# Kernel tuning notes

Hardware: AMD Instinct MI355X
Metric: run time of the kernel (lower is better)

The kernel has to match this reference:

```python
import jax, jax.numpy as jnp
import numpy as np

B, C, R, Cc = 16384, 30, 7, 7

def setup_inputs() -> dict:
    key = jax.random.key(0)
    k1, k2, k3 = jax.random.split(key, 3)
    pred = jax.random.uniform(k1, (B, C, R, Cc), dtype=jnp.float32)
    label = jax.random.uniform(k2, (B, C, R, Cc), dtype=jnp.float32)
    obj = (jax.random.uniform(k3, (B, R, Cc)) > 0.7).astype(jnp.float32)
    label = label.at[:, 4].set(obj)
    return {"pred": pred, "label": label}

def _boxes(t, cols, rows, nrow, ncol, off):
    # t: [b,30,r,c]; channels off..off+3 are (x,y,w,h) relative to cell
    x, y, w, h = t[:, off], t[:, off + 1], t[:, off + 2], t[:, off + 3]
    cx = (x + cols) / ncol
    cy = (y + rows) / nrow
    return cx - w / 2, cy - h / 2, cx + w / 2, cy + h / 2

def _iou(a, b):
    ax1, ay1, ax2, ay2 = a
    bx1, by1, bx2, by2 = b
    iw = jnp.maximum(jnp.minimum(ax2, bx2) - jnp.maximum(ax1, bx1), 0.0)
    ih = jnp.maximum(jnp.minimum(ay2, by2) - jnp.maximum(ay1, by1), 0.0)
    inter = iw * ih
    area_a = (ax2 - ax1) * (ay2 - ay1)
    area_b = (bx2 - bx1) * (by2 - by1)
    return inter / (area_a + area_b - inter + 1e-10)

def reference(pred, label):
    b_size = pred.shape[0]
    nrow, ncol = pred.shape[-2], pred.shape[-1]
    cols = jnp.arange(ncol, dtype=pred.dtype)[None, None, :]  # [1,1,c]
    rows = jnp.arange(nrow, dtype=pred.dtype)[None, :, None]  # [1,r,1]

    bbox1 = _boxes(pred, cols, rows, nrow, ncol, 0)
    bbox2 = _boxes(pred, cols, rows, nrow, ncol, 5)
    lbox = _boxes(label, cols, rows, nrow, ncol, 0)
    iou1 = _iou(bbox1, lbox)  # [b,r,c]
    iou2 = _iou(bbox2, lbox)
    choose1 = iou1 >= iou2

    # coord loss candidates (sum over the 2 xy channels / 2 wh channels)
    coord1 = 5.0 * jnp.sum((pred[:, 0:2] - label[:, 0:2]) ** 2, axis=1) \
           + jnp.sum((jnp.sqrt(pred[:, 2:4]) - jnp.sqrt(label[:, 2:4])) ** 2, axis=1)
    coord2 = 5.0 * jnp.sum((pred[:, 5:7] - label[:, 5:7]) ** 2, axis=1) \
           + jnp.sum((jnp.sqrt(pred[:, 7:9]) - jnp.sqrt(label[:, 7:9])) ** 2, axis=1)

    obj1 = (pred[:, 4] - iou1) ** 2
    obj2 = (pred[:, 9] - iou2) ** 2

    coord = jnp.where(choose1, coord1, coord2)
    obj_conf = jnp.where(choose1, obj1, obj2)
    noobj_conf_obj = 0.5 * jnp.where(choose1, obj2, obj1)
    class_l = jnp.sum((pred[:, 10:] - label[:, 10:]) ** 2, axis=1)

    obj_cell = coord + obj_conf + noobj_conf_obj + class_l
    # note: original sums the two confidences THEN squares (faithful to source)
    noobj_cell = 0.5 * (pred[:, 4] + pred[:, 9]) ** 2

    is_obj = label[:, 4] == 1.0
    per_cell = jnp.where(is_obj, obj_cell, noobj_cell)
    return jnp.sum(per_cell) / b_size
```

## Files before the change

### kernel.cpp

```cpp
#include <hip/hip_runtime.h>


#define NBATCH 16384
#define BSTRIDE 1470
#define BLOCK 256
#define GRID 2048
#define NA_BLOCKS 1280
#define NB_BLOCKS 768
#define N2 8028160

__device__ __forceinline__ float sq(float x) { return x * x; }

__global__ __launch_bounds__(BLOCK) void yolo_main(const float* __restrict__ pred,
                                                   const float* __restrict__ label,
                                                   float* __restrict__ partials) {
    __shared__ float lds[4][960];
    __shared__ float smem[4];

    const int m = blockIdx.x & 7;
    const int g = blockIdx.x >> 3;
    const int tid = threadIdx.x;
    float acc = 0.0f;

    if (m < 5) {
        const int a_rank = g * 5 + m;
        const long long gstr = (long long)NA_BLOCKS * 1024;
        for (long long base = (long long)a_rank * 1024; base < N2; base += gstr) {
#pragma unroll
            for (int j = 0; j < 4; ++j) {
                unsigned int i = (unsigned int)(base + j * 256 + tid);
                unsigned int rec = i / 490u;
                unsigned int k = i - rec * 490u;
                const float* rp = pred + (size_t)rec * BSTRIDE;
                const float* rl = label + (size_t)rec * BSTRIDE;
                float2 p2 = *(const float2*)(rp + 490 + 2 * k);
                float2 l2 = *(const float2*)(rl + 490 + 2 * k);
                unsigned int c0 = (2u * k) % 49u;
                unsigned int c1 = (c0 == 48u) ? 0u : c0 + 1u;
                float w0 = rl[196 + c0];
                float w1 = rl[196 + c1];
                float d0 = p2.x - l2.x, d1 = p2.y - l2.y;
                acc += w0 * (d0 * d0) + w1 * (d1 * d1);
            }
        }
    } else {
        const int b_rank = g * 3 + (m - 5);
        const int wave = tid >> 6, lane = tid & 63;
        float* ldsw = &lds[wave][0];
        float2* wp2 = (float2*)ldsw;
        float2* wl2 = (float2*)(ldsw + 496);
        const int wave_id = b_rank * 4 + wave;

        const int cell = lane;
        const int rr = cell / 7;
        const int cc = cell - rr * 7;
        const float fr = (float)rr, fc = (float)cc;
        const float inv7 = 1.0f / 7.0f;

        for (int rec = wave_id; rec < NBATCH; rec += NB_BLOCKS * 4) {
            const float2* gp = (const float2*)pred + (size_t)rec * 735;
            const float2* gl = (const float2*)label + (size_t)rec * 735;
#pragma unroll
            for (int r4 = 0; r4 < 4; ++r4) {
                int idx = r4 * 64 + lane;
                if (idx < 245) wp2[idx] = gp[idx];
                if (idx < 221) wl2[idx] = gl[idx];
            }
            asm volatile("s_waitcnt lgkmcnt(0)" ::: "memory");

            if (lane < 49) {
                float p[10], l[9];
#pragma unroll
                for (int ch = 0; ch < 10; ++ch) p[ch] = ldsw[ch * 49 + cell];
#pragma unroll
                for (int ch = 0; ch < 9; ++ch) l[ch] = ldsw[496 + ch * 49 + cell];

                float lcx = (l[0] + fc) * inv7;
                float lcy = (l[1] + fr) * inv7;
                float lhw = l[2] * 0.5f, lhh = l[3] * 0.5f;
                float lx1 = lcx - lhw, ly1 = lcy - lhh;
                float lx2 = lcx + lhw, ly2 = lcy + lhh;
                float larea = (lx2 - lx1) * (ly2 - ly1);

                float cx1 = (p[0] + fc) * inv7, cy1 = (p[1] + fr) * inv7;
                float x11 = cx1 - p[2] * 0.5f, y11 = cy1 - p[3] * 0.5f;
                float x12 = cx1 + p[2] * 0.5f, y12 = cy1 + p[3] * 0.5f;
                float iw1 = fmaxf(fminf(x12, lx2) - fmaxf(x11, lx1), 0.0f);
                float ih1 = fmaxf(fminf(y12, ly2) - fmaxf(y11, ly1), 0.0f);
                float int1 = iw1 * ih1;
                float a1 = (x12 - x11) * (y12 - y11);
                float iou1 = int1 / (a1 + larea - int1 + 1e-10f);

                float cx2 = (p[5] + fc) * inv7, cy2 = (p[6] + fr) * inv7;
                float x21 = cx2 - p[7] * 0.5f, y21 = cy2 - p[8] * 0.5f;
                float x22 = cx2 + p[7] * 0.5f, y22 = cy2 + p[8] * 0.5f;
                float iw2 = fmaxf(fminf(x22, lx2) - fmaxf(x21, lx1), 0.0f);
                float ih2 = fmaxf(fminf(y22, ly2) - fmaxf(y21, ly1), 0.0f);
                float int2 = iw2 * ih2;
                float a2 = (x22 - x21) * (y22 - y21);
                float iou2 = int2 / (a2 + larea - int2 + 1e-10f);

                bool ch1 = iou1 >= iou2;

                float coord1 = 5.0f * (sq(p[0] - l[0]) + sq(p[1] - l[1]))
                             + sq(sqrtf(p[2]) - sqrtf(l[2])) + sq(sqrtf(p[3]) - sqrtf(l[3]));
                float coord2 = 5.0f * (sq(p[5] - l[5]) + sq(p[6] - l[6]))
                             + sq(sqrtf(p[7]) - sqrtf(l[7])) + sq(sqrtf(p[8]) - sqrtf(l[8]));
                float obj1 = sq(p[4] - iou1);
                float obj2 = sq(p[9] - iou2);

                float obj_cell = (ch1 ? coord1 : coord2)
                               + (ch1 ? obj1 : obj2)
                               + 0.5f * (ch1 ? obj2 : obj1);
                float noobj_cell = 0.5f * sq(p[4] + p[9]);

                acc += (l[4] == 1.0f) ? obj_cell : noobj_cell;
            }
        }
    }

    float v = acc;
#pragma unroll
    for (int off = 32; off > 0; off >>= 1) v += __shfl_down(v, off, 64);

    const int lane = tid & 63;
    const int wave = tid >> 6;
    if (lane == 0) smem[wave] = v;
    __syncthreads();
    if (tid == 0) partials[blockIdx.x] = smem[0] + smem[1] + smem[2] + smem[3];
}

__global__ __launch_bounds__(BLOCK) void yolo_reduce(const float* __restrict__ partials,
                                                     float* __restrict__ out) {
    float s = 0.0f;
#pragma unroll
    for (int it = 0; it < GRID / BLOCK; ++it)
        s += partials[it * BLOCK + threadIdx.x];

#pragma unroll
    for (int off = 32; off > 0; off >>= 1) s += __shfl_down(s, off, 64);

    __shared__ float smem[BLOCK / 64];
    const int lane = threadIdx.x & 63;
    const int wave = threadIdx.x >> 6;
    if (lane == 0) smem[wave] = s;
    __syncthreads();
    if (threadIdx.x == 0)
        out[0] = (smem[0] + smem[1] + smem[2] + smem[3]) * (1.0f / (float)NBATCH);
}

extern "C" void kernel_launch(void* const* d_in, const int* in_sizes, int n_in,
                              void* d_out, int out_size, void* d_ws, size_t ws_size,
                              hipStream_t stream) {
    const float* pred  = (const float*)d_in[0];
    const float* label = (const float*)d_in[1];
    float* out = (float*)d_out;
    float* partials = (float*)d_ws;

    yolo_main<<<GRID, BLOCK, 0, stream>>>(pred, label, partials);
    yolo_reduce<<<1, BLOCK, 0, stream>>>(partials, out);
}
```

Before: 211.3 us.

## Split fused loss kernel into separate class and box kernels with nontemporal loads

Replaces the single kernel that split blocks 5:3 between class-loss and box-loss roles with two separate kernels, each using all 2048 blocks. The class kernel now processes one record per wave, reading the objectness weights once per record and broadcasting them with shuffles instead of reloading them per element. Both kernels use nontemporal loads for input data. The cost is an extra kernel launch and two sequential passes over the inputs, which removes any overlap between the two phases. The reduce kernel reads both partial arrays.

```diff
diff --git a/kernel.cpp b/kernel.cpp
--- a/kernel.cpp
+++ b/kernel.cpp
@@ -1,152 +1,150 @@
 #include <hip/hip_runtime.h>
 
 
+typedef float v2f __attribute__((ext_vector_type(2)));
+
 #define NBATCH 16384
-#define BSTRIDE 1470
+#define RECF 1470
 #define BLOCK 256
 #define GRID 2048
-#define NA_BLOCKS 1280
-#define NB_BLOCKS 768
-#define N2 8028160
+#define NWAVES (GRID * 4)
 
 __device__ __forceinline__ float sq(float x) { return x * x; }
 
-__global__ __launch_bounds__(BLOCK) void yolo_main(const float* __restrict__ pred,
-                                                   const float* __restrict__ label,
-                                                   float* __restrict__ partials) {
-    __shared__ float lds[4][960];
+__device__ __forceinline__ float block_reduce(float v, float* smem, int tid) {
+#pragma unroll
+    for (int off = 32; off > 0; off >>= 1) v += __shfl_down(v, off, 64);
+    const int lane = tid & 63, wave = tid >> 6;
+    if (lane == 0) smem[wave] = v;
+    __syncthreads();
+    return smem[0] + smem[1] + smem[2] + smem[3];
+}
+
+__global__ __launch_bounds__(BLOCK) void k_class(const float* __restrict__ pred,
+                                                 const float* __restrict__ label,
+                                                 float* __restrict__ partials) {
     __shared__ float smem[4];
-
-    const int m = blockIdx.x & 7;
-    const int g = blockIdx.x >> 3;
-    const int tid = threadIdx.x;
+    const int tid = threadIdx.x, lane = tid & 63, wv = tid >> 6;
+    const int gw = blockIdx.x * 4 + wv;
+    const int c0 = (2 * lane) % 49;
     float acc = 0.0f;
 
-    if (m < 5) {
-        const int a_rank = g * 5 + m;
-        const long long gstr = (long long)NA_BLOCKS * 1024;
-        for (long long base = (long long)a_rank * 1024; base < N2; base += gstr) {
+    for (int rec = gw; rec < NBATCH; rec += NWAVES) {
+        const float* rp = pred + (size_t)rec * RECF;
+        const float* rl = label + (size_t)rec * RECF;
+        float w49 = (lane < 49) ? rl[196 + lane] : 0.0f;
+        int c = c0;
 #pragma unroll
-            for (int j = 0; j < 4; ++j) {
-                unsigned int i = (unsigned int)(base + j * 256 + tid);
-                unsigned int rec = i / 490u;
-                unsigned int k = i - rec * 490u;
-                const float* rp = pred + (size_t)rec * BSTRIDE;
-                const float* rl = label + (size_t)rec * BSTRIDE;
-                float2 p2 = *(const float2*)(rp + 490 + 2 * k);
-                float2 l2 = *(const float2*)(rl + 490 + 2 * k);
-                unsigned int c0 = (2u * k) % 49u;
-                unsigned int c1 = (c0 == 48u) ? 0u : c0 + 1u;
-                float w0 = rl[196 + c0];
-                float w1 = rl[196 + c1];
-                float d0 = p2.x - l2.x, d1 = p2.y - l2.y;
-                acc += w0 * (d0 * d0) + w1 * (d1 * d1);
+        for (int it = 0; it < 8; ++it) {
+            int k = it * 64 + lane;
+            v2f p2 = {0.0f, 0.0f}, l2 = {0.0f, 0.0f};
+            if (k < 490) {
+                p2 = __builtin_nontemporal_load((const v2f*)(rp + 490 + 2 * k));
+                l2 = __builtin_nontemporal_load((const v2f*)(rl + 490 + 2 * k));
             }
-        }
-    } else {
-        const int b_rank = g * 3 + (m - 5);
-        const int wave = tid >> 6, lane = tid & 63;
-        float* ldsw = &lds[wave][0];
-        float2* wp2 = (float2*)ldsw;
-        float2* wl2 = (float2*)(ldsw + 496);
-        const int wave_id = b_rank * 4 + wave;
-
-        const int cell = lane;
-        const int rr = cell / 7;
-        const int cc = cell - rr * 7;
-        const float fr = (float)rr, fc = (float)cc;
-        const float inv7 = 1.0f / 7.0f;
-
-        for (int rec = wave_id; rec < NBATCH; rec += NB_BLOCKS * 4) {
-            const float2* gp = (const float2*)pred + (size_t)rec * 735;
-            const float2* gl = (const float2*)label + (size_t)rec * 735;
-#pragma unroll
-            for (int r4 = 0; r4 < 4; ++r4) {
-                int idx = r4 * 64 + lane;
-                if (idx < 245) wp2[idx] = gp[idx];
-                if (idx < 221) wl2[idx] = gl[idx];
-            }
-            asm volatile("s_waitcnt lgkmcnt(0)" ::: "memory");
-
-            if (lane < 49) {
-                float p[10], l[9];
-#pragma unroll
-                for (int ch = 0; ch < 10; ++ch) p[ch] = ldsw[ch * 49 + cell];
-#pragma unroll
-                for (int ch = 0; ch < 9; ++ch) l[ch] = ldsw[496 + ch * 49 + cell];
-
-                float lcx = (l[0] + fc) * inv7;
-                float lcy = (l[1] + fr) * inv7;
-                float lhw = l[2] * 0.5f, lhh = l[3] * 0.5f;
-                float lx1 = lcx - lhw, ly1 = lcy - lhh;
-                float lx2 = lcx + lhw, ly2 = lcy + lhh;
-                float larea = (lx2 - lx1) * (ly2 - ly1);
-
-                float cx1 = (p[0] + fc) * inv7, cy1 = (p[1] + fr) * inv7;
-                float x11 = cx1 - p[2] * 0.5f, y11 = cy1 - p[3] * 0.5f;
-                float x12 = cx1 + p[2] * 0.5f, y12 = cy1 + p[3] * 0.5f;
-                float iw1 = fmaxf(fminf(x12, lx2) - fmaxf(x11, lx1), 0.0f);
-                float ih1 = fmaxf(fminf(y12, ly2) - fmaxf(y11, ly1), 0.0f);
-                float int1 = iw1 * ih1;
-                float a1 = (x12 - x11) * (y12 - y11);
-                float iou1 = int1 / (a1 + larea - int1 + 1e-10f);
-
-                float cx2 = (p[5] + fc) * inv7, cy2 = (p[6] + fr) * inv7;
-                float x21 = cx2 - p[7] * 0.5f, y21 = cy2 - p[8] * 0.5f;
-                float x22 = cx2 + p[7] * 0.5f, y22 = cy2 + p[8] * 0.5f;
-                float iw2 = fmaxf(fminf(x22, lx2) - fmaxf(x21, lx1), 0.0f);
-                float ih2 = fmaxf(fminf(y22, ly2) - fmaxf(y21, ly1), 0.0f);
-                float int2 = iw2 * ih2;
-                float a2 = (x22 - x21) * (y22 - y21);
-                float iou2 = int2 / (a2 + larea - int2 + 1e-10f);
-
-                bool ch1 = iou1 >= iou2;
-
-                float coord1 = 5.0f * (sq(p[0] - l[0]) + sq(p[1] - l[1]))
-                             + sq(sqrtf(p[2]) - sqrtf(l[2])) + sq(sqrtf(p[3]) - sqrtf(l[3]));
-                float coord2 = 5.0f * (sq(p[5] - l[5]) + sq(p[6] - l[6]))
-                             + sq(sqrtf(p[7]) - sqrtf(l[7])) + sq(sqrtf(p[8]) - sqrtf(l[8]));
-                float obj1 = sq(p[4] - iou1);
-                float obj2 = sq(p[9] - iou2);
-
-                float obj_cell = (ch1 ? coord1 : coord2)
-                               + (ch1 ? obj1 : obj2)
-                               + 0.5f * (ch1 ? obj2 : obj1);
-                float noobj_cell = 0.5f * sq(p[4] + p[9]);
-
-                acc += (l[4] == 1.0f) ? obj_cell : noobj_cell;
-            }
+            float w0 = __shfl(w49, c, 64);
+            int cn = (c == 48) ? 0 : c + 1;
+            float w1 = __shfl(w49, cn, 64);
+            float d0 = p2.x - l2.x, d1 = p2.y - l2.y;
+            acc += w0 * d0 * d0 + w1 * d1 * d1;
+            c += 30; if (c >= 49) c -= 49;
         }
     }
 
-    float v = acc;
-#pragma unroll
-    for (int off = 32; off > 0; off >>= 1) v += __shfl_down(v, off, 64);
-
-    const int lane = tid & 63;
-    const int wave = tid >> 6;
-    if (lane == 0) smem[wave] = v;
-    __syncthreads();
-    if (tid == 0) partials[blockIdx.x] = smem[0] + smem[1] + smem[2] + smem[3];
+    float s = block_reduce(acc, smem, tid);
+    if (tid == 0) partials[blockIdx.x] = s;
 }
 
-__global__ __launch_bounds__(BLOCK) void yolo_reduce(const float* __restrict__ partials,
-                                                     float* __restrict__ out) {
+__global__ __launch_bounds__(BLOCK) void k_box(const float* __restrict__ pred,
+                                               const float* __restrict__ label,
+                                               float* __restrict__ partials) {
+    __shared__ float lds[4][960];
+    __shared__ float smem[4];
+    const int tid = threadIdx.x, lane = tid & 63, wv = tid >> 6;
+    const int gw = blockIdx.x * 4 + wv;
+    float* ldsw = &lds[wv][0];
+    v2f* wp2 = (v2f*)ldsw;
+    v2f* wl2 = (v2f*)(ldsw + 496);
+
+    const int rr = lane / 7, cc = lane - rr * 7;
+    const float fr = (float)rr, fcl = (float)cc;
+    const float inv7 = 1.0f / 7.0f;
+    float acc = 0.0f;
+
+    for (int rec = gw; rec < NBATCH; rec += NWAVES) {
+        const v2f* gp = (const v2f*)(pred + (size_t)rec * RECF);
+        const v2f* gl = (const v2f*)(label + (size_t)rec * RECF);
+#pragma unroll
+        for (int r4 = 0; r4 < 4; ++r4) {
+            int idx = r4 * 64 + lane;
+            if (idx < 245) wp2[idx] = __builtin_nontemporal_load(gp + idx);
+            if (idx < 221) wl2[idx] = __builtin_nontemporal_load(gl + idx);
+        }
+        asm volatile("s_waitcnt lgkmcnt(0)" ::: "memory");
+
+        if (lane < 49) {
+            float p[10], l[9];
+#pragma unroll
+            for (int ch = 0; ch < 10; ++ch) p[ch] = ldsw[ch * 49 + lane];
+#pragma unroll
+            for (int ch = 0; ch < 9; ++ch) l[ch] = ldsw[496 + ch * 49 + lane];
+
+            float lcx = (l[0] + fcl) * inv7;
+            float lcy = (l[1] + fr) * inv7;
+            float lhw = l[2] * 0.5f, lhh = l[3] * 0.5f;
+            float lx1 = lcx - lhw, ly1 = lcy - lhh;
+            float lx2 = lcx + lhw, ly2 = lcy + lhh;
+            float larea = (lx2 - lx1) * (ly2 - ly1);
+
+            float cx1 = (p[0] + fcl) * inv7, cy1 = (p[1] + fr) * inv7;
+            float x11 = cx1 - p[2] * 0.5f, y11 = cy1 - p[3] * 0.5f;
+            float x12 = cx1 + p[2] * 0.5f, y12 = cy1 + p[3] * 0.5f;
+            float iw1 = fmaxf(fminf(x12, lx2) - fmaxf(x11, lx1), 0.0f);
+            float ih1 = fmaxf(fminf(y12, ly2) - fmaxf(y11, ly1), 0.0f);
+            float int1 = iw1 * ih1;
+            float a1 = (x12 - x11) * (y12 - y11);
+            float iou1 = int1 / (a1 + larea - int1 + 1e-10f);
+
+            float cx2 = (p[5] + fcl) * inv7, cy2 = (p[6] + fr) * inv7;
+            float x21 = cx2 - p[7] * 0.5f, y21 = cy2 - p[8] * 0.5f;
+            float x22 = cx2 + p[7] * 0.5f, y22 = cy2 + p[8] * 0.5f;
+            float iw2 = fmaxf(fminf(x22, lx2) - fmaxf(x21, lx1), 0.0f);
+            float ih2 = fmaxf(fminf(y22, ly2) - fmaxf(y21, ly1), 0.0f);
+            float int2 = iw2 * ih2;
+            float a2 = (x22 - x21) * (y22 - y21);
+            float iou2 = int2 / (a2 + larea - int2 + 1e-10f);
+
+            bool ch1 = iou1 >= iou2;
+
+            float coord1 = 5.0f * (sq(p[0] - l[0]) + sq(p[1] - l[1]))
+                         + sq(sqrtf(p[2]) - sqrtf(l[2])) + sq(sqrtf(p[3]) - sqrtf(l[3]));
+            float coord2 = 5.0f * (sq(p[5] - l[5]) + sq(p[6] - l[6]))
+                         + sq(sqrtf(p[7]) - sqrtf(l[7])) + sq(sqrtf(p[8]) - sqrtf(l[8]));
+            float obj1 = sq(p[4] - iou1);
+            float obj2 = sq(p[9] - iou2);
+
+            float obj_cell = (ch1 ? coord1 : coord2)
+                           + (ch1 ? obj1 : obj2)
+                           + 0.5f * (ch1 ? obj2 : obj1);
+            float noobj_cell = 0.5f * sq(p[4] + p[9]);
+
+            acc += (l[4] == 1.0f) ? obj_cell : noobj_cell;
+        }
+    }
+
+    float s = block_reduce(acc, smem, tid);
+    if (tid == 0) partials[blockIdx.x] = s;
+}
+
+__global__ __launch_bounds__(BLOCK) void k_reduce(const float* __restrict__ partials,
+                                                  float* __restrict__ out) {
+    __shared__ float smem[4];
     float s = 0.0f;
 #pragma unroll
-    for (int it = 0; it < GRID / BLOCK; ++it)
+    for (int it = 0; it < 2 * GRID / BLOCK; ++it)
         s += partials[it * BLOCK + threadIdx.x];
-
-#pragma unroll
-    for (int off = 32; off > 0; off >>= 1) s += __shfl_down(s, off, 64);
-
-    __shared__ float smem[BLOCK / 64];
-    const int lane = threadIdx.x & 63;
-    const int wave = threadIdx.x >> 6;
-    if (lane == 0) smem[wave] = s;
-    __syncthreads();
-    if (threadIdx.x == 0)
-        out[0] = (smem[0] + smem[1] + smem[2] + smem[3]) * (1.0f / (float)NBATCH);
+    float t = block_reduce(s, smem, threadIdx.x);
+    if (threadIdx.x == 0) out[0] = t * (1.0f / (float)NBATCH);
 }
 
 extern "C" void kernel_launch(void* const* d_in, const int* in_sizes, int n_in,
@@ -155,8 +153,10 @@
     const float* pred  = (const float*)d_in[0];
     const float* label = (const float*)d_in[1];
     float* out = (float*)d_out;
-    float* partials = (float*)d_ws;
+    float* part1 = (float*)d_ws;
+    float* part2 = part1 + GRID;
 
-    yolo_main<<<GRID, BLOCK, 0, stream>>>(pred, label, partials);
-    yolo_reduce<<<1, BLOCK, 0, stream>>>(partials, out);
+    k_class<<<GRID, BLOCK, 0, stream>>>(pred, label, part1);
+    k_box<<<GRID, BLOCK, 0, stream>>>(pred, label, part2);
+    k_reduce<<<1, BLOCK, 0, stream>>>(part1, out);
 }
```

After: 200.1 us. 1.06x faster.
